# Optimization experiments

Hardware: AMD Instinct MI355X
Metric: run time of the kernel (lower is better)

The kernel has to match this reference:

```python
import jax, jax.numpy as jnp
import numpy as np

# (multiplicity, irrep dim 2l+1, is_scalar) for '128x0e + 64x1o + 32x2e'
IRREPS = [(128, 1, True), (64, 3, False), (32, 5, False)]
EPS = 1e-05
NUM_GRAPHS = 64


def setup_inputs() -> dict:
    key = jax.random.key(0)
    k1, k2 = jax.random.split(key)
    N, dim = 200000, 480
    x = jax.random.normal(k1, (N, dim), dtype=jnp.float32)
    batch_id = jnp.sort(jax.random.randint(k2, (N,), 0, NUM_GRAPHS)).astype(jnp.int64)
    weight = jnp.ones((224,), dtype=jnp.float32)   # per-irrep-channel scale
    bias = jnp.zeros((128,), dtype=jnp.float32)    # scalar channels only
    return {"input": x, "batch_id_tensor": batch_id, "weight": weight, "bias": bias}


def _segment_mean(vals, seg, num_segments):
    # vals: (N, mul) -> per-graph mean (G, mul)
    sums = jax.ops.segment_sum(vals, seg, num_segments=num_segments)
    counts = jax.ops.segment_sum(jnp.ones((vals.shape[0],), vals.dtype), seg,
                                 num_segments=num_segments)
    return sums / jnp.maximum(counts, 1.0)[:, None]


def reference(input, batch_id_tensor, weight, bias):
    N = input.shape[0]
    seg = batch_id_tensor.astype(jnp.int32)
    ix = iw = ib = 0
    outs = []
    for mul, d, is_scalar in IRREPS:
        f = input[:, ix:ix + mul * d].reshape(N, mul, d)
        ix += mul * d
        if is_scalar:
            # instance norm: per-graph mean of scalar channels, gathered back
            m = _segment_mean(f[:, :, 0], seg, NUM_GRAPHS)[seg]  # (N, mul)
            f = f - m[:, :, None]
        # 'component' normalization: mean of squares over irrep dim
        fn = jnp.mean(f * f, axis=2)                             # (N, mul)
        # reduce='mean' over (trivial) spatial axis, then per-graph mean
        fn = _segment_mean(fn, seg, NUM_GRAPHS)[seg]             # (N, mul)
        fn = (fn + EPS) ** -0.5 * weight[iw:iw + mul]
        iw += mul
        f = f * fn[:, :, None]
        if is_scalar:
            f = f + bias[ib:ib + mul][:, None]
            ib += mul
        outs.append(f.reshape(N, mul * d))
    return jnp.concatenate(outs, axis=1)
```

## Files before the change

### kernel.cpp

```cpp
#include <hip/hip_runtime.h>

#define NGRAPHS 64
#define DIM 480
#define NCH 224
#define EPS 1e-5f
#define TILE 128

typedef float f32x4 __attribute__((ext_vector_type(4)));

#define OFF_SSQ   0
#define OFF_SUM   14336
#define OFF_START 22528
#define OFF_TPRE  22593
#define ZN_FLOATS 22528

__device__ __forceinline__ int col2ch(int col) {
    if (col < 128) return col;
    if (col < 320) return 128 + (col - 128) / 3;
    return 192 + (col - 320) / 5;
}

__global__ __launch_bounds__(256) void init_kernel(const int* __restrict__ bid,
                                                   float* __restrict__ ws, int N) {
    int b = blockIdx.x;
    if (b < 88) {
        int i = b * 256 + threadIdx.x;
        if (i < ZN_FLOATS) ws[i] = 0.0f;
        return;
    }
    int* start = (int*)(ws + OFF_START);
    int* tpre  = (int*)(ws + OFF_TPRE);
    int g = threadIdx.x;
    if (g <= NGRAPHS) {
        int lo = 0, hi = N;
        while (lo < hi) {
            int mid = (lo + hi) >> 1;
            if (bid[mid] < g) lo = mid + 1; else hi = mid;
        }
        start[g] = lo;
    }
    __syncthreads();
    if (threadIdx.x == 0) {
        int acc = 0;
        for (int gg = 0; gg < NGRAPHS; ++gg) {
            tpre[gg] = acc;
            int cnt = start[gg + 1] - start[gg];
            acc += (cnt + TILE - 1) / TILE;
        }
        tpre[NGRAPHS] = acc;
    }
}

__device__ __forceinline__ void block_tile(const int* __restrict__ tpre, int b,
                                           int& g, int& tile) {
    int lo = 0, hi = NGRAPHS;
    while (hi - lo > 1) {
        int mid = (lo + hi) >> 1;
        if (tpre[mid] <= b) lo = mid; else hi = mid;
    }
    g = lo;
    tile = b - tpre[lo];
}

__device__ __forceinline__ void flush_quad(float* __restrict__ SQ, int col0,
                                           float v0, float v1, float v2, float v3) {
    float v[4] = {v0, v1, v2, v3};
    int ch0 = col2ch(col0), ch1 = col2ch(col0 + 1),
        ch2 = col2ch(col0 + 2), ch3 = col2ch(col0 + 3);
    float acc = v[0]; int cur = ch0;
    if (ch1 == cur) acc += v[1]; else { atomicAdd(&SQ[cur], acc); cur = ch1; acc = v[1]; }
    if (ch2 == cur) acc += v[2]; else { atomicAdd(&SQ[cur], acc); cur = ch2; acc = v[2]; }
    if (ch3 == cur) acc += v[3]; else { atomicAdd(&SQ[cur], acc); cur = ch3; acc = v[3]; }
    atomicAdd(&SQ[cur], acc);
}

__global__ __launch_bounds__(256) void stats_kernel(const float* __restrict__ x,
                                                    float* __restrict__ ws) {
    const int* start = (const int*)(ws + OFF_START);
    const int* tpre  = (const int*)(ws + OFF_TPRE);
    if ((int)blockIdx.x >= tpre[NGRAPHS]) return;
    int g, tile;
    block_tile(tpre, blockIdx.x, g, tile);
    int r0 = start[g] + tile * TILE;
    int r1 = min(r0 + TILE, start[g + 1]);

    const int tx = threadIdx.x & 63;
    const int ty = threadIdx.x >> 6;

    float ssq[8] = {0, 0, 0, 0, 0, 0, 0, 0};
    float ssum[4] = {0, 0, 0, 0};

    for (int r = r0 + ty; r < r1; r += 4) {
        const float4* rowp = (const float4*)(x + (size_t)r * DIM);
        float4 v0 = rowp[tx];
        ssq[0] += v0.x * v0.x; ssq[1] += v0.y * v0.y;
        ssq[2] += v0.z * v0.z; ssq[3] += v0.w * v0.w;
        if (tx < 32) {
            ssum[0] += v0.x; ssum[1] += v0.y; ssum[2] += v0.z; ssum[3] += v0.w;
        }
        if (tx < 56) {
            float4 v1 = rowp[64 + tx];
            ssq[4] += v1.x * v1.x; ssq[5] += v1.y * v1.y;
            ssq[6] += v1.z * v1.z; ssq[7] += v1.w * v1.w;
        }
    }

    __shared__ float red[256][12];
#pragma unroll
    for (int j = 0; j < 8; ++j) red[threadIdx.x][j] = ssq[j];
#pragma unroll
    for (int j = 0; j < 4; ++j) red[threadIdx.x][8 + j] = ssum[j];
    __syncthreads();

    if (ty == 0) {
        float s[8], sm[4];
#pragma unroll
        for (int j = 0; j < 8; ++j)
            s[j] = red[tx][j] + red[tx + 64][j] + red[tx + 128][j] + red[tx + 192][j];
#pragma unroll
        for (int j = 0; j < 4; ++j)
            sm[j] = red[tx][8 + j] + red[tx + 64][8 + j] + red[tx + 128][8 + j] + red[tx + 192][8 + j];

        float* SQ = ws + OFF_SSQ + (size_t)g * NCH;
        float* SM = ws + OFF_SUM + (size_t)g * 128;
        flush_quad(SQ, 4 * tx, s[0], s[1], s[2], s[3]);
        if (tx < 32) {
#pragma unroll
            for (int j = 0; j < 4; ++j) atomicAdd(&SM[4 * tx + j], sm[j]);
        }
        if (tx < 56) flush_quad(SQ, 256 + 4 * tx, s[4], s[5], s[6], s[7]);
    }
}

__global__ __launch_bounds__(256) void norm_kernel(const float* __restrict__ x,
                                                   const float* __restrict__ w,
                                                   const float* __restrict__ bias,
                                                   const float* __restrict__ ws,
                                                   float* __restrict__ out) {
    const int* start = (const int*)(ws + OFF_START);
    const int* tpre  = (const int*)(ws + OFF_TPRE);
    int total = tpre[NGRAPHS];
    int b = total - 1 - (int)blockIdx.x;
    if (b < 0) return;
    int t = threadIdx.x;
    if (t >= 240) return;
    int g, tile;
    block_tile(tpre, b, g, tile);
    int r0 = start[g] + tile * TILE;
    int r1 = min(r0 + TILE, start[g + 1]);

    int row_off = t / 120;
    int c4 = t - row_off * 120;

    float cnt = (float)max(start[g + 1] - start[g], 1);
    const float* SQ = ws + OFF_SSQ + (size_t)g * NCH;
    const float* SM = ws + OFF_SUM + (size_t)g * 128;

    float A[4], B[4];
#pragma unroll
    for (int j = 0; j < 4; ++j) {
        int col = 4 * c4 + j;
        int ch = col2ch(col);
        float ssq = SQ[ch];
        if (col < 128) {
            float m   = SM[col] / cnt;
            float var = ssq / cnt - m * m;
            float Av  = rsqrtf(var + EPS) * w[ch];
            A[j] = Av;
            B[j] = bias[col] - m * Av;
        } else {
            float d = (col < 320) ? 3.0f : 5.0f;
            A[j] = rsqrtf(ssq / (d * cnt) + EPS) * w[ch];
            B[j] = 0.0f;
        }
    }

    const float4* xp = (const float4*)(x + (size_t)(r0 + row_off) * DIM) + c4;
    float*        op = out + (size_t)(r0 + row_off) * DIM + 4 * c4;
    const int stride4 = 2 * (DIM / 4);
    const int strideF = 2 * DIM;
    for (int r = r0 + row_off; r < r1; r += 2) {
        float4 xv = *xp;
        f32x4 o;
        o.x = xv.x * A[0] + B[0];
        o.y = xv.y * A[1] + B[1];
        o.z = xv.z * A[2] + B[2];
        o.w = xv.w * A[3] + B[3];
        __builtin_nontemporal_store(o, (f32x4*)op);
        xp += stride4;
        op += strideF;
    }
}

extern "C" void kernel_launch(void* const* d_in, const int* in_sizes, int n_in,
                              void* d_out, int out_size, void* d_ws, size_t ws_size,
                              hipStream_t stream) {
    const float* x   = (const float*)d_in[0];
    const int*   bid = (const int*)d_in[1];
    const float* w   = (const float*)d_in[2];
    const float* b   = (const float*)d_in[3];
    float* ws  = (float*)d_ws;
    float* out = (float*)d_out;
    const int N = in_sizes[1];

    int max_tiles = (N + TILE - 1) / TILE + NGRAPHS;

    init_kernel<<<89, 256, 0, stream>>>(bid, ws, N);
    stats_kernel<<<max_tiles, 256, 0, stream>>>(x, ws);
    norm_kernel<<<max_tiles, 256, 0, stream>>>(x, w, b, ws, out);
}
```

Baseline: 257.1 us.

## Fuse init, stats and norm into one cooperative persistent kernel with grid syncs

Replaces the three separate launches (init, stats, norm) with a single cooperative kernel that loops persistently over tiles and uses grid-wide syncs between the zeroing, statistics and normalization phases. Each block recomputes the graph start offsets and tile prefix in shared memory instead of reading them from workspace. This aims to remove launch gaps and inter-kernel drain. In exchange it adds grid-sync cost and persistent-loop scheduling. The old three-kernel path is kept as a fallback if the cooperative launch fails.

```diff
diff --git a/kernel.cpp b/kernel.cpp
--- a/kernel.cpp
+++ b/kernel.cpp
@@ -1,10 +1,14 @@
 #include <hip/hip_runtime.h>
+#include <hip/hip_cooperative_groups.h>
+
+namespace cg = cooperative_groups;
 
 #define NGRAPHS 64
 #define DIM 480
 #define NCH 224
 #define EPS 1e-5f
 #define TILE 128
+#define NCU 256
 
 typedef float f32x4 __attribute__((ext_vector_type(4)));
 
@@ -18,48 +22,6 @@
     if (col < 128) return col;
     if (col < 320) return 128 + (col - 128) / 3;
     return 192 + (col - 320) / 5;
-}
-
-__global__ __launch_bounds__(256) void init_kernel(const int* __restrict__ bid,
-                                                   float* __restrict__ ws, int N) {
-    int b = blockIdx.x;
-    if (b < 88) {
-        int i = b * 256 + threadIdx.x;
-        if (i < ZN_FLOATS) ws[i] = 0.0f;
-        return;
-    }
-    int* start = (int*)(ws + OFF_START);
-    int* tpre  = (int*)(ws + OFF_TPRE);
-    int g = threadIdx.x;
-    if (g <= NGRAPHS) {
-        int lo = 0, hi = N;
-        while (lo < hi) {
-            int mid = (lo + hi) >> 1;
-            if (bid[mid] < g) lo = mid + 1; else hi = mid;
-        }
-        start[g] = lo;
-    }
-    __syncthreads();
-    if (threadIdx.x == 0) {
-        int acc = 0;
-        for (int gg = 0; gg < NGRAPHS; ++gg) {
-            tpre[gg] = acc;
-            int cnt = start[gg + 1] - start[gg];
-            acc += (cnt + TILE - 1) / TILE;
-        }
-        tpre[NGRAPHS] = acc;
-    }
-}
-
-__device__ __forceinline__ void block_tile(const int* __restrict__ tpre, int b,
-                                           int& g, int& tile) {
-    int lo = 0, hi = NGRAPHS;
-    while (hi - lo > 1) {
-        int mid = (lo + hi) >> 1;
-        if (tpre[mid] <= b) lo = mid; else hi = mid;
-    }
-    g = lo;
-    tile = b - tpre[lo];
 }
 
 __device__ __forceinline__ void flush_quad(float* __restrict__ SQ, int col0,
@@ -74,8 +36,197 @@
     atomicAdd(&SQ[cur], acc);
 }
 
+
+__device__ __forceinline__ void stats_tile(const float* __restrict__ x, int g,
+                                           int r0, int r1, int tx, int ty, int t,
+                                           float (*red)[13], float* __restrict__ ws) {
+    float ssq[8]  = {0, 0, 0, 0, 0, 0, 0, 0};
+    float ssum[4] = {0, 0, 0, 0};
+    for (int r = r0 + ty; r < r1; r += 4) {
+        const float4* rowp = (const float4*)(x + (size_t)r * DIM);
+        float4 v0 = rowp[tx];
+        ssq[0] += v0.x * v0.x; ssq[1] += v0.y * v0.y;
+        ssq[2] += v0.z * v0.z; ssq[3] += v0.w * v0.w;
+        if (tx < 32) { ssum[0] += v0.x; ssum[1] += v0.y; ssum[2] += v0.z; ssum[3] += v0.w; }
+        if (tx < 56) {
+            float4 v1 = rowp[64 + tx];
+            ssq[4] += v1.x * v1.x; ssq[5] += v1.y * v1.y;
+            ssq[6] += v1.z * v1.z; ssq[7] += v1.w * v1.w;
+        }
+    }
+#pragma unroll
+    for (int j = 0; j < 8; ++j) red[t][j] = ssq[j];
+#pragma unroll
+    for (int j = 0; j < 4; ++j) red[t][8 + j] = ssum[j];
+    __syncthreads();
+    if (ty == 0) {
+        float s[8], sm[4];
+#pragma unroll
+        for (int j = 0; j < 8; ++j)
+            s[j] = red[tx][j] + red[tx + 64][j] + red[tx + 128][j] + red[tx + 192][j];
+#pragma unroll
+        for (int j = 0; j < 4; ++j)
+            sm[j] = red[tx][8 + j] + red[tx + 64][8 + j] + red[tx + 128][8 + j] + red[tx + 192][8 + j];
+        float* SQ = ws + OFF_SSQ + (size_t)g * NCH;
+        float* SM = ws + OFF_SUM + (size_t)g * 128;
+        flush_quad(SQ, 4 * tx, s[0], s[1], s[2], s[3]);
+        if (tx < 32) {
+#pragma unroll
+            for (int j = 0; j < 4; ++j) atomicAdd(&SM[4 * tx + j], sm[j]);
+        }
+        if (tx < 56) flush_quad(SQ, 256 + 4 * tx, s[4], s[5], s[6], s[7]);
+    }
+    __syncthreads();
+}
+
+__device__ __forceinline__ void norm_tile(const float* __restrict__ x,
+                                          const float* __restrict__ w,
+                                          const float* __restrict__ bias,
+                                          const float* __restrict__ ws,
+                                          float* __restrict__ out,
+                                          int g, int r0, int r1, int cnt_rows,
+                                          int row_off, int c4) {
+    float cnt = (float)max(cnt_rows, 1);
+    const float* SQ = ws + OFF_SSQ + (size_t)g * NCH;
+    const float* SM = ws + OFF_SUM + (size_t)g * 128;
+    float A[4], B[4];
+#pragma unroll
+    for (int j = 0; j < 4; ++j) {
+        int col = 4 * c4 + j;
+        int ch = col2ch(col);
+        float ssq = SQ[ch];
+        if (col < 128) {
+            float m   = SM[col] / cnt;
+            float var = ssq / cnt - m * m;
+            float Av  = rsqrtf(var + EPS) * w[ch];
+            A[j] = Av;
+            B[j] = bias[col] - m * Av;
+        } else {
+            float d = (col < 320) ? 3.0f : 5.0f;
+            A[j] = rsqrtf(ssq / (d * cnt) + EPS) * w[ch];
+            B[j] = 0.0f;
+        }
+    }
+    const float4* xp = (const float4*)(x + (size_t)(r0 + row_off) * DIM) + c4;
+    float*        op = out + (size_t)(r0 + row_off) * DIM + 4 * c4;
+    const int stride4 = 2 * (DIM / 4);
+    const int strideF = 2 * DIM;
+    for (int r = r0 + row_off; r < r1; r += 2) {
+        float4 xv = *xp;
+        f32x4 o;
+        o.x = xv.x * A[0] + B[0];
+        o.y = xv.y * A[1] + B[1];
+        o.z = xv.z * A[2] + B[2];
+        o.w = xv.w * A[3] + B[3];
+        __builtin_nontemporal_store(o, (f32x4*)op);
+        xp += stride4;
+        op += strideF;
+    }
+}
+
+
+__global__ __launch_bounds__(256, 4) void fused_kernel(
+        const float* __restrict__ x, const int* __restrict__ bid,
+        const float* __restrict__ w, const float* __restrict__ bias,
+        float* __restrict__ ws, float* __restrict__ out, int N) {
+    __shared__ int s_start[NGRAPHS + 1];
+    __shared__ int s_tpre[NGRAPHS + 1];
+    __shared__ float red[256][13];
+
+    const int t  = threadIdx.x;
+    const int tx = t & 63;
+    const int ty = t >> 6;
+
+    if (t <= NGRAPHS) {
+        int g = t, lo = 0, hi = N;
+        while (lo < hi) { int mid = (lo + hi) >> 1; if (bid[mid] < g) lo = mid + 1; else hi = mid; }
+        s_start[g] = lo;
+    }
+    for (int i = blockIdx.x * 256 + t; i < ZN_FLOATS; i += gridDim.x * 256)
+        ws[i] = 0.0f;
+    __syncthreads();
+    if (t == 0) {
+        int acc = 0;
+        for (int g = 0; g < NGRAPHS; ++g) {
+            s_tpre[g] = acc;
+            acc += (s_start[g + 1] - s_start[g] + TILE - 1) / TILE;
+        }
+        s_tpre[NGRAPHS] = acc;
+    }
+    __syncthreads();
+    const int ntiles = s_tpre[NGRAPHS];
+
+    cg::this_grid().sync();
+
+    for (int b = blockIdx.x; b < ntiles; b += gridDim.x) {
+        int lo = 0, hi = NGRAPHS;
+        while (hi - lo > 1) { int mid = (lo + hi) >> 1; if (s_tpre[mid] <= b) lo = mid; else hi = mid; }
+        int g  = lo;
+        int r0 = s_start[g] + (b - s_tpre[g]) * TILE;
+        int r1 = min(r0 + TILE, s_start[g + 1]);
+        stats_tile(x, g, r0, r1, tx, ty, t, red, ws);
+    }
+
+    cg::this_grid().sync();
+
+    const int row_off = t / 120;
+    const int c4 = t - row_off * 120;
+    for (int k = blockIdx.x; k < ntiles; k += gridDim.x) {
+        int b = ntiles - 1 - k;
+        if (t < 240) {
+            int lo = 0, hi = NGRAPHS;
+            while (hi - lo > 1) { int mid = (lo + hi) >> 1; if (s_tpre[mid] <= b) lo = mid; else hi = mid; }
+            int g  = lo;
+            int r0 = s_start[g] + (b - s_tpre[g]) * TILE;
+            int r1 = min(r0 + TILE, s_start[g + 1]);
+            norm_tile(x, w, bias, ws, out, g, r0, r1,
+                      s_start[g + 1] - s_start[g], row_off, c4);
+        }
+    }
+}
+
+
+__global__ __launch_bounds__(256) void init_kernel(const int* __restrict__ bid,
+                                                   float* __restrict__ ws, int N) {
+    int b = blockIdx.x;
+    if (b < 88) {
+        int i = b * 256 + threadIdx.x;
+        if (i < ZN_FLOATS) ws[i] = 0.0f;
+        return;
+    }
+    int* start = (int*)(ws + OFF_START);
+    int* tpre  = (int*)(ws + OFF_TPRE);
+    int g = threadIdx.x;
+    if (g <= NGRAPHS) {
+        int lo = 0, hi = N;
+        while (lo < hi) { int mid = (lo + hi) >> 1; if (bid[mid] < g) lo = mid + 1; else hi = mid; }
+        start[g] = lo;
+    }
+    __syncthreads();
+    if (threadIdx.x == 0) {
+        int acc = 0;
+        for (int gg = 0; gg < NGRAPHS; ++gg) {
+            tpre[gg] = acc;
+            acc += (start[gg + 1] - start[gg] + TILE - 1) / TILE;
+        }
+        tpre[NGRAPHS] = acc;
+    }
+}
+
+__device__ __forceinline__ void block_tile(const int* __restrict__ tpre, int b,
+                                           int& g, int& tile) {
+    int lo = 0, hi = NGRAPHS;
+    while (hi - lo > 1) {
+        int mid = (lo + hi) >> 1;
+        if (tpre[mid] <= b) lo = mid; else hi = mid;
+    }
+    g = lo;
+    tile = b - tpre[lo];
+}
+
 __global__ __launch_bounds__(256) void stats_kernel(const float* __restrict__ x,
                                                     float* __restrict__ ws) {
+    __shared__ float red[256][13];
     const int* start = (const int*)(ws + OFF_START);
     const int* tpre  = (const int*)(ws + OFF_TPRE);
     if ((int)blockIdx.x >= tpre[NGRAPHS]) return;
@@ -83,53 +234,7 @@
     block_tile(tpre, blockIdx.x, g, tile);
     int r0 = start[g] + tile * TILE;
     int r1 = min(r0 + TILE, start[g + 1]);
-
-    const int tx = threadIdx.x & 63;
-    const int ty = threadIdx.x >> 6;
-
-    float ssq[8] = {0, 0, 0, 0, 0, 0, 0, 0};
-    float ssum[4] = {0, 0, 0, 0};
-
-    for (int r = r0 + ty; r < r1; r += 4) {
-        const float4* rowp = (const float4*)(x + (size_t)r * DIM);
-        float4 v0 = rowp[tx];
-        ssq[0] += v0.x * v0.x; ssq[1] += v0.y * v0.y;
-        ssq[2] += v0.z * v0.z; ssq[3] += v0.w * v0.w;
-        if (tx < 32) {
-            ssum[0] += v0.x; ssum[1] += v0.y; ssum[2] += v0.z; ssum[3] += v0.w;
-        }
-        if (tx < 56) {
-            float4 v1 = rowp[64 + tx];
-            ssq[4] += v1.x * v1.x; ssq[5] += v1.y * v1.y;
-            ssq[6] += v1.z * v1.z; ssq[7] += v1.w * v1.w;
-        }
-    }
-
-    __shared__ float red[256][12];
-#pragma unroll
-    for (int j = 0; j < 8; ++j) red[threadIdx.x][j] = ssq[j];
-#pragma unroll
-    for (int j = 0; j < 4; ++j) red[threadIdx.x][8 + j] = ssum[j];
-    __syncthreads();
-
-    if (ty == 0) {
-        float s[8], sm[4];
-#pragma unroll
-        for (int j = 0; j < 8; ++j)
-            s[j] = red[tx][j] + red[tx + 64][j] + red[tx + 128][j] + red[tx + 192][j];
-#pragma unroll
-        for (int j = 0; j < 4; ++j)
-            sm[j] = red[tx][8 + j] + red[tx + 64][8 + j] + red[tx + 128][8 + j] + red[tx + 192][8 + j];
-
-        float* SQ = ws + OFF_SSQ + (size_t)g * NCH;
-        float* SM = ws + OFF_SUM + (size_t)g * 128;
-        flush_quad(SQ, 4 * tx, s[0], s[1], s[2], s[3]);
-        if (tx < 32) {
-#pragma unroll
-            for (int j = 0; j < 4; ++j) atomicAdd(&SM[4 * tx + j], sm[j]);
-        }
-        if (tx < 56) flush_quad(SQ, 256 + 4 * tx, s[4], s[5], s[6], s[7]);
-    }
+    stats_tile(x, g, r0, r1, threadIdx.x & 63, threadIdx.x >> 6, threadIdx.x, red, ws);
 }
 
 __global__ __launch_bounds__(256) void norm_kernel(const float* __restrict__ x,
@@ -148,48 +253,8 @@
     block_tile(tpre, b, g, tile);
     int r0 = start[g] + tile * TILE;
     int r1 = min(r0 + TILE, start[g + 1]);
-
-    int row_off = t / 120;
-    int c4 = t - row_off * 120;
-
-    float cnt = (float)max(start[g + 1] - start[g], 1);
-    const float* SQ = ws + OFF_SSQ + (size_t)g * NCH;
-    const float* SM = ws + OFF_SUM + (size_t)g * 128;
-
-    float A[4], B[4];
-#pragma unroll
-    for (int j = 0; j < 4; ++j) {
-        int col = 4 * c4 + j;
-        int ch = col2ch(col);
-        float ssq = SQ[ch];
-        if (col < 128) {
-            float m   = SM[col] / cnt;
-            float var = ssq / cnt - m * m;
-            float Av  = rsqrtf(var + EPS) * w[ch];
-            A[j] = Av;
-            B[j] = bias[col] - m * Av;
-        } else {
-            float d = (col < 320) ? 3.0f : 5.0f;
-            A[j] = rsqrtf(ssq / (d * cnt) + EPS) * w[ch];
-            B[j] = 0.0f;
-        }
-    }
-
-    const float4* xp = (const float4*)(x + (size_t)(r0 + row_off) * DIM) + c4;
-    float*        op = out + (size_t)(r0 + row_off) * DIM + 4 * c4;
-    const int stride4 = 2 * (DIM / 4);
-    const int strideF = 2 * DIM;
-    for (int r = r0 + row_off; r < r1; r += 2) {
-        float4 xv = *xp;
-        f32x4 o;
-        o.x = xv.x * A[0] + B[0];
-        o.y = xv.y * A[1] + B[1];
-        o.z = xv.z * A[2] + B[2];
-        o.w = xv.w * A[3] + B[3];
-        __builtin_nontemporal_store(o, (f32x4*)op);
-        xp += stride4;
-        op += strideF;
-    }
+    norm_tile(x, w, bias, ws, out, g, r0, r1, start[g + 1] - start[g],
+              t / 120, t % 120);
 }
 
 extern "C" void kernel_launch(void* const* d_in, const int* in_sizes, int n_in,
@@ -201,11 +266,22 @@
     const float* b   = (const float*)d_in[3];
     float* ws  = (float*)d_ws;
     float* out = (float*)d_out;
-    const int N = in_sizes[1];
-
-    int max_tiles = (N + TILE - 1) / TILE + NGRAPHS;
-
-    init_kernel<<<89, 256, 0, stream>>>(bid, ws, N);
-    stats_kernel<<<max_tiles, 256, 0, stream>>>(x, ws);
-    norm_kernel<<<max_tiles, 256, 0, stream>>>(x, w, b, ws, out);
-}
+    int N = in_sizes[1];
+    int ntiles_ub = (N + TILE - 1) / TILE + NGRAPHS;
+
+    int maxb = 0;
+    if (hipOccupancyMaxActiveBlocksPerMultiprocessor(&maxb, fused_kernel, 256, 0) != hipSuccess
+        || maxb < 1) maxb = 1;
+    int grid = maxb * NCU;
+    if (grid > ntiles_ub) grid = ntiles_ub;
+
+    void* args[] = {(void*)&x, (void*)&bid, (void*)&w, (void*)&b,
+                    (void*)&ws, (void*)&out, (void*)&N};
+    hipError_t e = hipLaunchCooperativeKernel((const void*)fused_kernel, dim3(grid),
+                                              dim3(256), args, 0, stream);
+    if (e != hipSuccess) {
+        init_kernel<<<89, 256, 0, stream>>>(bid, ws, N);
+        stats_kernel<<<ntiles_ub, 256, 0, stream>>>(x, ws);
+        norm_kernel<<<ntiles_ub, 256, 0, stream>>>(x, w, b, ws, out);
+    }
+}
```

After: 427.1 us. 66.2% more time.
